# Performance work log

Hardware: AMD Instinct MI355X
Metric: run time of the kernel (lower is better)

The kernel has to match this reference:

```python
import jax, jax.numpy as jnp
import numpy as np

INPUT_SIZE = 512
OUTPUT_SIZE = 512
BATCH = 65536
HIDDEN = [256, 128, 64, 32]


def _linear_params(key, fan_in, fan_out):
    # torch nn.Linear default init: U(-1/sqrt(fan_in), 1/sqrt(fan_in))
    kw, kb = jax.random.split(key)
    bound = 1.0 / np.sqrt(fan_in)
    w = jax.random.uniform(kw, (fan_out, fan_in), jnp.float32, -bound, bound)
    b = jax.random.uniform(kb, (fan_out,), jnp.float32, -bound, bound)
    return w, b


def setup_inputs() -> dict:
    key = jax.random.key(0)
    ks = jax.random.split(key, 6)
    x = jax.random.normal(ks[0], (BATCH, INPUT_SIZE), jnp.float32)
    dims = [INPUT_SIZE] + HIDDEN + [OUTPUT_SIZE]
    inp = {"x": x}
    for i in range(5):
        w, b = _linear_params(ks[i + 1], dims[i], dims[i + 1])
        inp[f"w{i+1}"] = w
        inp[f"b{i+1}"] = b
    return inp


def reference(x, w1, b1, w2, b2, w3, b3, w4, b4, w5, b5):
    sig = jax.nn.sigmoid
    # in_size = number of nonzero entries in row 0 (replaces per-element python loop)
    in_size = jnp.count_nonzero(x[0])  # traced int scalar
    h = sig(x @ w1.T + b1)
    h = sig(h @ w2.T + b2)
    h = sig(h @ w3.T + b3)
    h = sig(h @ w4.T + b4)
    y = h @ w5.T + b5  # [B, OUTPUT_SIZE]
    # out has shape [B, INPUT_SIZE]; out[:, :in_size] = y[:, :in_size]
    # (INPUT_SIZE == OUTPUT_SIZE here, so a prefix mask suffices)
    mask = jnp.arange(INPUT_SIZE) < in_size  # [INPUT_SIZE]
    out = jnp.where(mask[None, :], y, jnp.zeros((), y.dtype))
    return out
```

## Files before the change

### kernel.cpp

```cpp
#include <hip/hip_runtime.h>
#include <hip/hip_bf16.h>
#include <stdint.h>

typedef __attribute__((ext_vector_type(4))) float f32x4;
typedef __attribute__((ext_vector_type(4))) unsigned int u32x4;
typedef __attribute__((ext_vector_type(8))) short short8;

#define MFMA16(a, b, c) __builtin_amdgcn_mfma_f32_16x16x32_bf16((a), (b), (c), 0, 0, 0)

__device__ __forceinline__ uint16_t f2bf(float f) {
  __hip_bfloat16 h = __float2bfloat16(f);
  return __builtin_bit_cast(uint16_t, h);
}

__device__ __forceinline__ float fast_sigmoid(float v) {
  return __builtin_amdgcn_rcpf(1.f + __expf(-v));
}

__device__ __forceinline__ short8 cvt8(f32x4 a, f32x4 b) {
  short8 r;
  r[0] = (short)f2bf(a[0]); r[1] = (short)f2bf(a[1]);
  r[2] = (short)f2bf(a[2]); r[3] = (short)f2bf(a[3]);
  r[4] = (short)f2bf(b[0]); r[5] = (short)f2bf(b[1]);
  r[6] = (short)f2bf(b[2]); r[7] = (short)f2bf(b[3]);
  return r;
}

template <int RB>
__device__ __forceinline__ int swzoff(int row, int bcol) {
  constexpr int SLM = (((RB / 16) < 8 ? (RB / 16) : 8)) - 1;
  return row * RB + (bcol ^ ((row & SLM) << 4));
}

template <int RB>
__device__ __forceinline__ short8 lds_a(const uint16_t* buf, int row0, int k0, int lane) {
  int r = row0 + (lane & 15);
  int bcol = (k0 + ((lane >> 4) << 3)) * 2;
  u32x4 raw = *(const u32x4*)((const char*)buf + swzoff<RB>(r, bcol));
  return __builtin_bit_cast(short8, raw);
}

__device__ __forceinline__ short8 lds_a144(const char* sb, int row0, int kk, int lane) {
  int r = row0 + (lane & 15);
  return *(const short8*)(sb + r * 144 + ((kk * 4 + (lane >> 4)) << 4));
}

__device__ __forceinline__ short8 load_frag_f32(const float* M, int ld, int r0, int k0, int lane) {
  const float* p = M + (size_t)(r0 + (lane & 15)) * ld + (k0 + ((lane >> 4) << 3));
  f32x4 a = *(const f32x4*)p;
  f32x4 b = *(const f32x4*)(p + 4);
  return cvt8(a, b);
}

__device__ __forceinline__ short8 load_b_pk(const char* base, int f, int lane) {
  u32x4 raw = *(const u32x4*)(base + (((size_t)f * 64 + lane) << 4));
  return __builtin_bit_cast(short8, raw);
}

template <bool P>
__device__ __forceinline__ short8 bfrag(const char* wp, const float* W, int K,
                                        int f0, int ntg, int KT, int kt, int lane) {
  if constexpr (P) {
    return load_b_pk(wp, f0 + ntg * KT + kt, lane);
  } else {
    return load_frag_f32(W, K, ntg * 16, kt * 32, lane);
  }
}

__global__ void pack_kernel(const float* __restrict__ w1, const float* __restrict__ w2,
                            const float* __restrict__ w3, const float* __restrict__ w4,
                            const float* __restrict__ w5, char* __restrict__ ws) {
  int b = blockIdx.x, lane = threadIdx.x;
  const float* W;
  int K, f0;
  if (b < 256)      { W = w1; K = 512; f0 = 0; }
  else if (b < 320) { W = w2; K = 256; f0 = 256; }
  else if (b < 336) { W = w3; K = 128; f0 = 320; }
  else if (b < 340) { W = w4; K = 64;  f0 = 336; }
  else              { W = w5; K = 32;  f0 = 340; }
  int f = b - f0;
  int KT = K / 32;
  int nt = f / KT, kt = f % KT;
  short8 r = load_frag_f32(W, K, nt * 16, kt * 32, lane);
  *(u32x4*)(ws + (((size_t)b * 64 + lane) << 4)) = __builtin_bit_cast(u32x4, r);
}

#define CHUNK_BAR()                                           \
  asm volatile("s_waitcnt lgkmcnt(0)" ::: "memory");          \
  __builtin_amdgcn_s_barrier();                               \
  __builtin_amdgcn_sched_barrier(0);

#define KSTEP64(C)                                                            \
  {                                                                           \
    CHUNK_BAR();                                                              \
    if ((C) + 2 < 8) {                                                        \
      const float* p = xrow + ((C) + 2) * 64;                                 \
      rA[(C) & 1][0] = *(const f32x4*)p;                                      \
      rA[(C) & 1][1] = *(const f32x4*)(p + 4);                                \
      rA[(C) & 1][2] = *(const f32x4*)(p + 32);                               \
      rA[(C) & 1][3] = *(const f32x4*)(p + 36);                               \
    }                                                                         \
    if ((C) + 1 < 8) {                                                        \
      short8 wv0 = cvt8(rA[((C) + 1) & 1][0], rA[((C) + 1) & 1][1]);          \
      short8 wv1 = cvt8(rA[((C) + 1) & 1][2], rA[((C) + 1) & 1][3]);          \
      char* wb = sring + (((C) + 1) & 1) * 9216 + swb;                        \
      *(short8*)(wb) = wv0;                                                   \
      *(short8*)(wb + 64) = wv1;                                              \
    }                                                                         \
    const char* sc = sring + ((C) & 1) * 9216;                                \
    _Pragma("unroll") for (int m = 0; m < 4; ++m) {                           \
      short8 a = lds_a144(sc, m * 16, 0, lane);                               \
      _Pragma("unroll") for (int nt = 0; nt < 4; ++nt)                        \
          acc[m][nt] = MFMA16(a, bfr[0][nt], acc[m][nt]);                     \
    }                                                                         \
    if (2 * (C) + 2 < 16) {                                                   \
      _Pragma("unroll") for (int nt = 0; nt < 4; ++nt)                        \
          bfr[0][nt] =                                                        \
              bfrag<P>(wp, w1, 512, 0, wid * 4 + nt, 16, 2 * (C) + 2, lane);  \
    }                                                                         \
    _Pragma("unroll") for (int m = 0; m < 4; ++m) {                           \
      short8 a = lds_a144(sc, m * 16, 1, lane);                               \
      _Pragma("unroll") for (int nt = 0; nt < 4; ++nt)                        \
          acc[m][nt] = MFMA16(a, bfr[1][nt], acc[m][nt]);                     \
    }                                                                         \
    if (2 * (C) + 3 < 16) {                                                   \
      _Pragma("unroll") for (int nt = 0; nt < 4; ++nt)                        \
          bfr[1][nt] =                                                        \
              bfrag<P>(wp, w1, 512, 0, wid * 4 + nt, 16, 2 * (C) + 3, lane);  \
    }                                                                         \
  }

template <bool P>
__global__ __launch_bounds__(256, 3) void mlp5_kernel(
    const float* __restrict__ x,
    const float* __restrict__ w1, const float* __restrict__ b1,
    const float* __restrict__ w2, const float* __restrict__ b2,
    const float* __restrict__ w3, const float* __restrict__ b3,
    const float* __restrict__ w4, const float* __restrict__ b4,
    const float* __restrict__ w5, const float* __restrict__ b5,
    const char* __restrict__ wp, float* __restrict__ out) {
  __shared__ __align__(16) char smem[32 * 1024];
  uint16_t* H1 = (uint16_t*)smem;
  uint16_t* H2 = (uint16_t*)smem;
  uint16_t* H3 = (uint16_t*)(smem + 16 * 1024);
  uint16_t* H4 = (uint16_t*)(smem + 24 * 1024);

  const int tid = threadIdx.x;
  const int lane = tid & 63;
  const int wid = tid >> 6;
  const int row0 = blockIdx.x * 64;
  const int lr = (lane >> 4) << 2;
  const int lc = lane & 15;

  int in_size = 0;
#pragma unroll
  for (int j = 0; j < 8; ++j) {
    float v = x[j * 64 + lane];
    in_size += (int)__popcll(__ballot(v != 0.f));
  }

  char* sring = smem;
  const float* xrow =
      x + (size_t)(row0 + wid * 16 + (lane & 15)) * 512 + ((lane >> 4) << 3);
  const int swb = (wid * 16 + (lane & 15)) * 144 + ((lane >> 4) << 4);

  f32x4 acc[4][4];
#pragma unroll
  for (int m = 0; m < 4; ++m)
#pragma unroll
    for (int n = 0; n < 4; ++n) acc[m][n] = (f32x4){0.f, 0.f, 0.f, 0.f};

  f32x4 rA[2][4];
  short8 bfr[2][4];
  rA[0][0] = *(const f32x4*)(xrow + 0);
  rA[0][1] = *(const f32x4*)(xrow + 4);
  rA[0][2] = *(const f32x4*)(xrow + 32);
  rA[0][3] = *(const f32x4*)(xrow + 36);
  rA[1][0] = *(const f32x4*)(xrow + 64);
  rA[1][1] = *(const f32x4*)(xrow + 68);
  rA[1][2] = *(const f32x4*)(xrow + 96);
  rA[1][3] = *(const f32x4*)(xrow + 100);
#pragma unroll
  for (int nt = 0; nt < 4; ++nt)
    bfr[0][nt] = bfrag<P>(wp, w1, 512, 0, wid * 4 + nt, 16, 0, lane);
#pragma unroll
  for (int nt = 0; nt < 4; ++nt)
    bfr[1][nt] = bfrag<P>(wp, w1, 512, 0, wid * 4 + nt, 16, 1, lane);
  {
    short8 wv0 = cvt8(rA[0][0], rA[0][1]);
    short8 wv1 = cvt8(rA[0][2], rA[0][3]);
    *(short8*)(sring + swb) = wv0;
    *(short8*)(sring + swb + 64) = wv1;
  }

  KSTEP64(0) KSTEP64(1) KSTEP64(2) KSTEP64(3)
  KSTEP64(4) KSTEP64(5) KSTEP64(6) KSTEP64(7)

  short8 bfr2[2][8];
#pragma unroll
  for (int n = 0; n < 2; ++n)
#pragma unroll
    for (int kt = 0; kt < 8; ++kt)
      bfr2[n][kt] = bfrag<P>(wp, w2, 256, 256, wid * 2 + n, 8, kt, lane);
  float bv1[4];
#pragma unroll
  for (int n = 0; n < 4; ++n) bv1[n] = b1[wid * 64 + n * 16 + lc];

  __syncthreads();

#pragma unroll
  for (int n = 0; n < 4; ++n) {
    const int ncol = wid * 64 + n * 16;
#pragma unroll
    for (int m = 0; m < 4; ++m)
#pragma unroll
      for (int i = 0; i < 4; ++i) {
        float v = fast_sigmoid(acc[m][n][i] + bv1[n]);
        *(uint16_t*)((char*)H1 + swzoff<512>(m * 16 + lr + i, (ncol + lc) * 2)) = f2bf(v);
      }
  }
  __syncthreads();

  {
    f32x4 acc2[4][2];
#pragma unroll
    for (int m = 0; m < 4; ++m)
#pragma unroll
      for (int n = 0; n < 2; ++n) acc2[m][n] = (f32x4){0.f, 0.f, 0.f, 0.f};
#pragma unroll
    for (int m = 0; m < 4; ++m) {
#pragma unroll
      for (int kt = 0; kt < 8; ++kt) {
        short8 afr = lds_a<512>(H1, m * 16, kt * 32, lane);
        acc2[m][0] = MFMA16(afr, bfr2[0][kt], acc2[m][0]);
        acc2[m][1] = MFMA16(afr, bfr2[1][kt], acc2[m][1]);
      }
    }
    short8 bfr3[4];
#pragma unroll
    for (int kt = 0; kt < 4; ++kt)
      bfr3[kt] = bfrag<P>(wp, w3, 128, 320, wid, 4, kt, lane);
    float bv2[2];
#pragma unroll
    for (int n = 0; n < 2; ++n) bv2[n] = b2[wid * 32 + n * 16 + lc];
    __syncthreads();
#pragma unroll
    for (int n = 0; n < 2; ++n) {
      const int ncol = wid * 32 + n * 16;
#pragma unroll
      for (int m = 0; m < 4; ++m)
#pragma unroll
        for (int i = 0; i < 4; ++i) {
          float v = fast_sigmoid(acc2[m][n][i] + bv2[n]);
          *(uint16_t*)((char*)H2 + swzoff<256>(m * 16 + lr + i, (ncol + lc) * 2)) = f2bf(v);
        }
    }
    __syncthreads();

    f32x4 acc3[4];
#pragma unroll
    for (int m = 0; m < 4; ++m) acc3[m] = (f32x4){0.f, 0.f, 0.f, 0.f};
#pragma unroll
    for (int m = 0; m < 4; ++m)
#pragma unroll
      for (int kt = 0; kt < 4; ++kt) {
        short8 afr = lds_a<256>(H2, m * 16, kt * 32, lane);
        acc3[m] = MFMA16(afr, bfr3[kt], acc3[m]);
      }
    short8 bfr4[2];
#pragma unroll
    for (int kt = 0; kt < 2; ++kt)
      bfr4[kt] = bfrag<P>(wp, w4, 64, 336, wid & 1, 2, kt, lane);
    const float bv3 = b3[wid * 16 + lc];
    {
#pragma unroll
      for (int m = 0; m < 4; ++m)
#pragma unroll
        for (int i = 0; i < 4; ++i) {
          float v = fast_sigmoid(acc3[m][i] + bv3);
          *(uint16_t*)((char*)H3 + swzoff<128>(m * 16 + lr + i, (wid * 16 + lc) * 2)) = f2bf(v);
        }
    }
    __syncthreads();

    const int wm = wid >> 1, wn = wid & 1;
    f32x4 acc4[2];
#pragma unroll
    for (int mt = 0; mt < 2; ++mt) acc4[mt] = (f32x4){0.f, 0.f, 0.f, 0.f};
#pragma unroll
    for (int mt = 0; mt < 2; ++mt)
#pragma unroll
      for (int kt = 0; kt < 2; ++kt) {
        short8 afr = lds_a<128>(H3, wm * 32 + mt * 16, kt * 32, lane);
        acc4[mt] = MFMA16(afr, bfr4[kt], acc4[mt]);
      }
    short8 bfr5[8];
#pragma unroll
    for (int nt = 0; nt < 8; ++nt)
      bfr5[nt] = bfrag<P>(wp, w5, 32, 340, wid * 8 + nt, 1, 0, lane);
    const float bv4 = b4[wn * 16 + lc];
    float bv5[8];
#pragma unroll
    for (int nt = 0; nt < 8; ++nt) bv5[nt] = b5[wid * 128 + nt * 16 + lc];
    {
#pragma unroll
      for (int mt = 0; mt < 2; ++mt)
#pragma unroll
        for (int i = 0; i < 4; ++i) {
          float v = fast_sigmoid(acc4[mt][i] + bv4);
          *(uint16_t*)((char*)H4 + swzoff<64>(wm * 32 + mt * 16 + lr + i, (wn * 16 + lc) * 2)) = f2bf(v);
        }
    }
    __syncthreads();

#pragma unroll
    for (int m = 0; m < 4; ++m) {
      short8 afr = lds_a<64>(H4, m * 16, 0, lane);
#pragma unroll
      for (int nt = 0; nt < 8; ++nt) {
        f32x4 av = MFMA16(afr, bfr5[nt], ((f32x4){0.f, 0.f, 0.f, 0.f}));
        const int col = wid * 128 + nt * 16 + lc;
        const bool keep = col < in_size;
#pragma unroll
        for (int i = 0; i < 4; ++i) {
          float v = keep ? (av[i] + bv5[nt]) : 0.f;
          out[(size_t)(row0 + m * 16 + lr + i) * 512 + col] = v;
        }
      }
    }
  }
}

extern "C" void kernel_launch(void* const* d_in, const int* in_sizes, int n_in,
                              void* d_out, int out_size, void* d_ws, size_t ws_size,
                              hipStream_t stream) {
  const float* x  = (const float*)d_in[0];
  const float* w1 = (const float*)d_in[1];
  const float* b1 = (const float*)d_in[2];
  const float* w2 = (const float*)d_in[3];
  const float* b2 = (const float*)d_in[4];
  const float* w3 = (const float*)d_in[5];
  const float* b3 = (const float*)d_in[6];
  const float* w4 = (const float*)d_in[7];
  const float* b4 = (const float*)d_in[8];
  const float* w5 = (const float*)d_in[9];
  const float* b5 = (const float*)d_in[10];
  float* out = (float*)d_out;

  dim3 grid(65536 / 64);
  dim3 block(256);
  const bool packed = ws_size >= (size_t)(372 * 1024);
  if (packed) {
    pack_kernel<<<372, 64, 0, stream>>>(w1, w2, w3, w4, w5, (char*)d_ws);
    mlp5_kernel<true><<<grid, block, 0, stream>>>(x, w1, b1, w2, b2, w3, b3, w4, b4,
                                                  w5, b5, (const char*)d_ws, out);
  } else {
    mlp5_kernel<false><<<grid, block, 0, stream>>>(x, w1, b1, w2, b2, w3, b3, w4, b4,
                                                   w5, b5, nullptr, out);
  }
}
```

Baseline: 76.15 us.

## Halve block row tile to 32 rows, doubling grid and shrinking LDS

Each block now handles 32 batch rows instead of 64. Accumulators, the staging ring and all per-layer M loops are halved, and the x load mapping is remapped so each lane loads 8 floats per chunk. This cuts LDS to 16KB and register pressure, which should allow more resident blocks and better latency hiding. The cost is that every block reloads the full weight fragments for half as many rows, doubling weight traffic and per-block overhead.

Result: no change. 75.29 us (-1.1%).

```diff
diff --git a/kernel.cpp b/kernel.cpp
--- a/kernel.cpp
+++ b/kernel.cpp
@@ -97,18 +97,13 @@
       const float* p = xrow + ((C) + 2) * 64;                                 \
       rA[(C) & 1][0] = *(const f32x4*)p;                                      \
       rA[(C) & 1][1] = *(const f32x4*)(p + 4);                                \
-      rA[(C) & 1][2] = *(const f32x4*)(p + 32);                               \
-      rA[(C) & 1][3] = *(const f32x4*)(p + 36);                               \
     }                                                                         \
     if ((C) + 1 < 8) {                                                        \
-      short8 wv0 = cvt8(rA[((C) + 1) & 1][0], rA[((C) + 1) & 1][1]);          \
-      short8 wv1 = cvt8(rA[((C) + 1) & 1][2], rA[((C) + 1) & 1][3]);          \
-      char* wb = sring + (((C) + 1) & 1) * 9216 + swb;                        \
-      *(short8*)(wb) = wv0;                                                   \
-      *(short8*)(wb + 64) = wv1;                                              \
-    }                                                                         \
-    const char* sc = sring + ((C) & 1) * 9216;                                \
-    _Pragma("unroll") for (int m = 0; m < 4; ++m) {                           \
+      short8 wv = cvt8(rA[((C) + 1) & 1][0], rA[((C) + 1) & 1][1]);           \
+      *(short8*)(sring + (((C) + 1) & 1) * 4608 + swb) = wv;                  \
+    }                                                                         \
+    const char* sc = sring + ((C) & 1) * 4608;                                \
+    _Pragma("unroll") for (int m = 0; m < 2; ++m) {                           \
       short8 a = lds_a144(sc, m * 16, 0, lane);                               \
       _Pragma("unroll") for (int nt = 0; nt < 4; ++nt)                        \
           acc[m][nt] = MFMA16(a, bfr[0][nt], acc[m][nt]);                     \
@@ -118,7 +113,7 @@
           bfr[0][nt] =                                                        \
               bfrag<P>(wp, w1, 512, 0, wid * 4 + nt, 16, 2 * (C) + 2, lane);  \
     }                                                                         \
-    _Pragma("unroll") for (int m = 0; m < 4; ++m) {                           \
+    _Pragma("unroll") for (int m = 0; m < 2; ++m) {                           \
       short8 a = lds_a144(sc, m * 16, 1, lane);                               \
       _Pragma("unroll") for (int nt = 0; nt < 4; ++nt)                        \
           acc[m][nt] = MFMA16(a, bfr[1][nt], acc[m][nt]);                     \
@@ -139,16 +134,16 @@
     const float* __restrict__ w4, const float* __restrict__ b4,
     const float* __restrict__ w5, const float* __restrict__ b5,
     const char* __restrict__ wp, float* __restrict__ out) {
-  __shared__ __align__(16) char smem[32 * 1024];
+  __shared__ __align__(16) char smem[16 * 1024];
   uint16_t* H1 = (uint16_t*)smem;
   uint16_t* H2 = (uint16_t*)smem;
-  uint16_t* H3 = (uint16_t*)(smem + 16 * 1024);
-  uint16_t* H4 = (uint16_t*)(smem + 24 * 1024);
+  uint16_t* H3 = (uint16_t*)(smem + 8 * 1024);
+  uint16_t* H4 = (uint16_t*)(smem + 12 * 1024);
 
   const int tid = threadIdx.x;
   const int lane = tid & 63;
   const int wid = tid >> 6;
-  const int row0 = blockIdx.x * 64;
+  const int row0 = blockIdx.x * 32;
   const int lr = (lane >> 4) << 2;
   const int lc = lane & 15;
 
@@ -161,25 +156,21 @@
 
   char* sring = smem;
   const float* xrow =
-      x + (size_t)(row0 + wid * 16 + (lane & 15)) * 512 + ((lane >> 4) << 3);
-  const int swb = (wid * 16 + (lane & 15)) * 144 + ((lane >> 4) << 4);
-
-  f32x4 acc[4][4];
-#pragma unroll
-  for (int m = 0; m < 4; ++m)
+      x + (size_t)(row0 + wid * 8 + (lane >> 3)) * 512 + ((lane & 7) << 3);
+  const int swb = (wid * 8 + (lane >> 3)) * 144 + ((lane & 7) << 4);
+
+  f32x4 acc[2][4];
+#pragma unroll
+  for (int m = 0; m < 2; ++m)
 #pragma unroll
     for (int n = 0; n < 4; ++n) acc[m][n] = (f32x4){0.f, 0.f, 0.f, 0.f};
 
-  f32x4 rA[2][4];
+  f32x4 rA[2][2];
   short8 bfr[2][4];
   rA[0][0] = *(const f32x4*)(xrow + 0);
   rA[0][1] = *(const f32x4*)(xrow + 4);
-  rA[0][2] = *(const f32x4*)(xrow + 32);
-  rA[0][3] = *(const f32x4*)(xrow + 36);
   rA[1][0] = *(const f32x4*)(xrow + 64);
   rA[1][1] = *(const f32x4*)(xrow + 68);
-  rA[1][2] = *(const f32x4*)(xrow + 96);
-  rA[1][3] = *(const f32x4*)(xrow + 100);
 #pragma unroll
   for (int nt = 0; nt < 4; ++nt)
     bfr[0][nt] = bfrag<P>(wp, w1, 512, 0, wid * 4 + nt, 16, 0, lane);
@@ -187,10 +178,8 @@
   for (int nt = 0; nt < 4; ++nt)
     bfr[1][nt] = bfrag<P>(wp, w1, 512, 0, wid * 4 + nt, 16, 1, lane);
   {
-    short8 wv0 = cvt8(rA[0][0], rA[0][1]);
-    short8 wv1 = cvt8(rA[0][2], rA[0][3]);
-    *(short8*)(sring + swb) = wv0;
-    *(short8*)(sring + swb + 64) = wv1;
+    short8 wv = cvt8(rA[0][0], rA[0][1]);
+    *(short8*)(sring + swb) = wv;
   }
 
   KSTEP64(0) KSTEP64(1) KSTEP64(2) KSTEP64(3)
@@ -212,7 +201,7 @@
   for (int n = 0; n < 4; ++n) {
     const int ncol = wid * 64 + n * 16;
 #pragma unroll
-    for (int m = 0; m < 4; ++m)
+    for (int m = 0; m < 2; ++m)
 #pragma unroll
       for (int i = 0; i < 4; ++i) {
         float v = fast_sigmoid(acc[m][n][i] + bv1[n]);
@@ -222,13 +211,13 @@
   __syncthreads();
 
   {
-    f32x4 acc2[4][2];
-#pragma unroll
-    for (int m = 0; m < 4; ++m)
+    f32x4 acc2[2][2];
+#pragma unroll
+    for (int m = 0; m < 2; ++m)
 #pragma unroll
       for (int n = 0; n < 2; ++n) acc2[m][n] = (f32x4){0.f, 0.f, 0.f, 0.f};
 #pragma unroll
-    for (int m = 0; m < 4; ++m) {
+    for (int m = 0; m < 2; ++m) {
 #pragma unroll
       for (int kt = 0; kt < 8; ++kt) {
         short8 afr = lds_a<512>(H1, m * 16, kt * 32, lane);
@@ -248,7 +237,7 @@
     for (int n = 0; n < 2; ++n) {
       const int ncol = wid * 32 + n * 16;
 #pragma unroll
-      for (int m = 0; m < 4; ++m)
+      for (int m = 0; m < 2; ++m)
 #pragma unroll
         for (int i = 0; i < 4; ++i) {
           float v = fast_sigmoid(acc2[m][n][i] + bv2[n]);
@@ -257,11 +246,11 @@
     }
     __syncthreads();
 
-    f32x4 acc3[4];
-#pragma unroll
-    for (int m = 0; m < 4; ++m) acc3[m] = (f32x4){0.f, 0.f, 0.f, 0.f};
-#pragma unroll
-    for (int m = 0; m < 4; ++m)
+    f32x4 acc3[2];
+#pragma unroll
+    for (int m = 0; m < 2; ++m) acc3[m] = (f32x4){0.f, 0.f, 0.f, 0.f};
+#pragma unroll
+    for (int m = 0; m < 2; ++m)
 #pragma unroll
       for (int kt = 0; kt < 4; ++kt) {
         short8 afr = lds_a<256>(H2, m * 16, kt * 32, lane);
@@ -274,7 +263,7 @@
     const float bv3 = b3[wid * 16 + lc];
     {
 #pragma unroll
-      for (int m = 0; m < 4; ++m)
+      for (int m = 0; m < 2; ++m)
 #pragma unroll
         for (int i = 0; i < 4; ++i) {
           float v = fast_sigmoid(acc3[m][i] + bv3);
@@ -284,16 +273,12 @@
     __syncthreads();
 
     const int wm = wid >> 1, wn = wid & 1;
-    f32x4 acc4[2];
-#pragma unroll
-    for (int mt = 0; mt < 2; ++mt) acc4[mt] = (f32x4){0.f, 0.f, 0.f, 0.f};
-#pragma unroll
-    for (int mt = 0; mt < 2; ++mt)
-#pragma unroll
-      for (int kt = 0; kt < 2; ++kt) {
-        short8 afr = lds_a<128>(H3, wm * 32 + mt * 16, kt * 32, lane);
-        acc4[mt] = MFMA16(afr, bfr4[kt], acc4[mt]);
-      }
+    f32x4 acc4 = (f32x4){0.f, 0.f, 0.f, 0.f};
+#pragma unroll
+    for (int kt = 0; kt < 2; ++kt) {
+      short8 afr = lds_a<128>(H3, wm * 16, kt * 32, lane);
+      acc4 = MFMA16(afr, bfr4[kt], acc4);
+    }
     short8 bfr5[8];
 #pragma unroll
     for (int nt = 0; nt < 8; ++nt)
@@ -304,17 +289,15 @@
     for (int nt = 0; nt < 8; ++nt) bv5[nt] = b5[wid * 128 + nt * 16 + lc];
     {
 #pragma unroll
-      for (int mt = 0; mt < 2; ++mt)
-#pragma unroll
-        for (int i = 0; i < 4; ++i) {
-          float v = fast_sigmoid(acc4[mt][i] + bv4);
-          *(uint16_t*)((char*)H4 + swzoff<64>(wm * 32 + mt * 16 + lr + i, (wn * 16 + lc) * 2)) = f2bf(v);
-        }
+      for (int i = 0; i < 4; ++i) {
+        float v = fast_sigmoid(acc4[i] + bv4);
+        *(uint16_t*)((char*)H4 + swzoff<64>(wm * 16 + lr + i, (wn * 16 + lc) * 2)) = f2bf(v);
+      }
     }
     __syncthreads();
 
 #pragma unroll
-    for (int m = 0; m < 4; ++m) {
+    for (int m = 0; m < 2; ++m) {
       short8 afr = lds_a<64>(H4, m * 16, 0, lane);
 #pragma unroll
       for (int nt = 0; nt < 8; ++nt) {
@@ -347,7 +330,7 @@
   const float* b5 = (const float*)d_in[10];
   float* out = (float*)d_out;
 
-  dim3 grid(65536 / 64);
+  dim3 grid(65536 / 32);
   dim3 block(256);
   const bool packed = ws_size >= (size_t)(372 * 1024);
   if (packed) {
```
